# Kernel optimization log

Measured on AMD Instinct MI355X. Metric: run time of the kernel, lower is better.

Reference implementation:

```python
import jax, jax.numpy as jnp
import numpy as np

EPS = 2e-05
N_H_RDG = 9   # lifting scale grid: h_j = 2**j, j=0..8
N_H_CROP = 3  # group-conv scale support: offsets 0,1,2 (dyadic index shifts)


def _scaled_kernel(w, h):
    """Resample base kernel w [O, I, K] (taps on integers centered at 0) at
    coordinates x/h via linear interpolation -> [O, I, (K-1)*h+1], with the
    R+ Haar-measure normalization 1/h (psi_h(x) = psi(x/h)/h)."""
    K = w.shape[-1]
    Kh = (K - 1) * h + 1
    m = jnp.arange(K, dtype=jnp.float32) - K // 2
    x = (jnp.arange(Kh, dtype=jnp.float32) - Kh // 2) / h
    hat = jnp.maximum(0.0, 1.0 - jnp.abs(x[:, None] - m[None, :]))  # [Kh, K]
    return jnp.einsum('oim,xm->oix', w, hat) / h


def _conv1d_same(x, k):
    pad = (k.shape[-1] - 1) // 2
    return jax.lax.conv_general_dilated(
        x, k, window_strides=(1,), padding=[(pad, pad)],
        dimension_numbers=('NCH', 'OIH', 'NCH'))


def _pool_r1(x, stride):
    # max pool over the spatial (last) axis only: kernel 4, pad 1 each side
    return jax.lax.reduce_window(
        x, -jnp.inf, jax.lax.max,
        window_dimensions=(1, 1, 1, 4), window_strides=(1, 1, 1, stride),
        padding=((0, 0), (0, 0), (0, 0), (1, 1)))


def _bn(x, g, b):
    # BatchNorm2d over [B, C, H_scale, L], training-mode batch stats
    mu = jnp.mean(x, axis=(0, 2, 3), keepdims=True)
    var = jnp.var(x, axis=(0, 2, 3), keepdims=True)
    return (x - mu) * jax.lax.rsqrt(var + EPS) * g[None, :, None, None] + b[None, :, None, None]


def _forward(x, w1, w2, w3, g1, b1, g2, b2, g3, b3, fw1, fb1, fw2, fb2, fw3, fb3):
    B = x.shape[0]
    # --- c1: GConvRdG lifting, scales h_j = 2**j, j=0..8 ---
    out = jnp.stack([_conv1d_same(x, _scaled_kernel(w1, 2 ** j))
                     for j in range(N_H_RDG)], axis=2)      # [B,16,9,16]
    out = _bn(jax.nn.relu(_pool_r1(out, 2)), g1, b1)        # [B,16,9,8]
    # --- c2: GConvGG, h_crop=True: out scale j uses in scales j..j+2 ---
    O2, I2 = w2.shape[0], w2.shape[1]
    w2r = w2.reshape(O2, I2 * N_H_CROP, 3)
    H2 = out.shape[2] - (N_H_CROP - 1)  # 7
    out = jnp.stack([
        _conv1d_same(out[:, :, j:j + N_H_CROP, :].reshape(B, I2 * N_H_CROP, -1),
                     _scaled_kernel(w2r, 2 ** j))
        for j in range(H2)], axis=2)                        # [B,32,7,8]
    out = _bn(jax.nn.relu(_pool_r1(out, 2)), g2, b2)        # [B,32,7,4]
    # --- c3: GConvGG with 1x1 spatial kernel ---
    w3s = w3[:, :, :, 0]  # [64,32,3]
    H3 = out.shape[2] - (N_H_CROP - 1)  # 5
    out = jnp.stack([
        jnp.einsum('oik,bikl->bol', w3s, out[:, :, j:j + N_H_CROP, :]) / (2.0 ** j)
        for j in range(H3)], axis=2)                        # [B,64,5,4]
    out = _bn(jax.nn.relu(_pool_r1(out, 4)), g3, b3)        # [B,64,5,1]
    # --- MLP head (dropout is identity in eval) ---
    out = out.reshape(B, -1)                                # [B,320]
    out = out @ fw1.T + fb1
    out = out @ fw2.T + fb2
    return out @ fw3.T + fb3                                # [B,17]


def setup_inputs() -> dict:
    key = jax.random.key(0)
    ks = jax.random.split(key, 7)
    B = 4096
    x = jax.random.normal(ks[0], (B, 6, 16), dtype=jnp.float32)
    w1 = jax.random.normal(ks[1], (16, 6, 7), dtype=jnp.float32) * (6 * 7) ** -0.5
    w2 = jax.random.normal(ks[2], (32, 16, 3, 3), dtype=jnp.float32) * (16 * 3 * 3) ** -0.5
    w3 = jax.random.normal(ks[3], (64, 32, 3, 1), dtype=jnp.float32) * (32 * 3) ** -0.5
    fw1 = jax.random.normal(ks[4], (16, 320), dtype=jnp.float32) * 320 ** -0.5
    fw2 = jax.random.normal(ks[5], (16, 16), dtype=jnp.float32) * 16 ** -0.5
    fw3 = jax.random.normal(ks[6], (17, 16), dtype=jnp.float32) * 16 ** -0.5
    return {
        'x': x, 'w1': w1, 'w2': w2, 'w3': w3,
        'g1': jnp.ones(16), 'b1': jnp.zeros(16),
        'g2': jnp.ones(32), 'b2': jnp.zeros(32),
        'g3': jnp.ones(64), 'b3': jnp.zeros(64),
        'fw1': fw1, 'fb1': jnp.zeros(16),
        'fw2': fw2, 'fb2': jnp.zeros(16),
        'fw3': fw3, 'fb3': jnp.zeros(17),
    }


def reference(x, w1, w2, w3, g1, b1, g2, b2, g3, b3, fw1, fb1, fw2, fb2, fw3, fb3):
    return _forward(x, w1, w2, w3, g1, b1, g2, b2, g3, b3, fw1, fb1, fw2, fb2, fw3, fb3)
```

## Files before the change

### kernel.cpp

```cpp
#include <hip/hip_runtime.h>

#define EPS 2e-5f

using short8  = __attribute__((ext_vector_type(8))) short;
using floatx4 = __attribute__((ext_vector_type(4))) float;

static __device__ inline unsigned short f2bf(float f) {
    unsigned u = __float_as_uint(f);
    u += 0x7fffu + ((u >> 16) & 1u);
    return (unsigned short)(u >> 16);
}
static __device__ inline float bf2f(short s) {
    return __uint_as_float(((unsigned)(unsigned short)s) << 16);
}
static __device__ inline short8 scale8(short8 v, float sc) {
    short8 r;
    #pragma unroll
    for (int e = 0; e < 8; ++e) r[e] = (short)f2bf(bf2f(v[e]) * sc);
    return r;
}


__global__ void __launch_bounds__(256) kSa(const float* __restrict__ w1,
                                           unsigned short* __restrict__ W1f,
                                           float* __restrict__ stats) {
    int gid = blockIdx.x * 256 + threadIdx.x;
    if (gid < 256) stats[gid] = 0.f;
    int j  = gid / 24576;
    int r  = gid % 24576;
    int T  = r / 1536;
    int r2 = r % 1536;
    int ks = r2 / 512;
    int r3 = r2 % 512;
    int ln = r3 >> 3, e = r3 & 7;
    int n  = T * 16 + (ln & 15);
    int kk = ks * 32 + (ln >> 4) * 8 + e;
    int o = n >> 4, t = n & 15;
    int i = kk >> 4, s = kk & 15;
    int h = 1 << j;
    int d = s - t;
    float val = 0.f;
    if (d >= -3 * h && d <= 3 * h) {
        float df = (float)d / (float)h;
        #pragma unroll
        for (int m = 0; m < 7; ++m) {
            float hat = fmaxf(0.f, 1.f - fabsf(df - (float)(m - 3)));
            val += w1[(o * 6 + i) * 7 + m] * hat;
        }
        val /= (float)h;
    }
    W1f[gid] = f2bf(val);
}

__global__ void __launch_bounds__(256) k1(const float* __restrict__ x,
                                          const unsigned short* __restrict__ W1f,
                                          const float* __restrict__ w2,
                                          const float* __restrict__ w3,
                                          const float* __restrict__ fw1,
                                          unsigned short* __restrict__ p1,
                                          unsigned short* __restrict__ W2r,
                                          float* __restrict__ S,
                                          float* __restrict__ W3fF,
                                          float* __restrict__ W1rF,
                                          float* __restrict__ stats1, int B) {
    __shared__ float z[32 * 276];
    __shared__ float lsS[256], lsQ[256];
    int tid = threadIdx.x;

    if (blockIdx.y == 9) {
        int base = blockIdx.x * 256 + tid;
        for (int g = base; g < 688128; g += 32768) {
            int fs = g >> 9;
            int ln = (g >> 3) & 63, e = g & 7;
            int j  = fs / 192;
            int rm = fs % 192;
            int T  = rm / 12, ks = rm % 12;
            int col = T * 16 + (ln & 15);
            int k   = ks * 32 + (ln >> 4) * 8 + e;
            int o = col >> 3, t = col & 7;
            int ic = k >> 3, s = k & 7;
            int i = ic / 3, c = ic % 3;
            int h = 1 << j;
            int d = s - t;
            float raw = 0.f;
            if (d >= -h && d <= h) {
                float df = (float)d / (float)h;
                #pragma unroll
                for (int m = 0; m < 3; ++m) {
                    float hat = fmaxf(0.f, 1.f - fabsf(df - (float)(m - 1)));
                    raw += w2[((o * 16 + i) * 3 + c) * 3 + m] * hat;
                }
                raw /= (float)h;
            }
            W2r[g] = f2bf(raw);
        }
        for (int g = base; g < 28672; g += 32768) {
            int j = g >> 12;
            int r = g & 4095;
            int i = r >> 8;
            int col = r & 255;
            int o = col >> 3, t = col & 7;
            int h = 1 << j;
            float acc = 0.f;
            #pragma unroll
            for (int c = 0; c < 3; ++c) {
                const float* wr = &w2[((o * 16 + i) * 3 + c) * 3];
                #pragma unroll
                for (int s = 0; s < 8; ++s) {
                    int d = s - t;
                    if (d >= -h && d <= h) {
                        float df = (float)d / (float)h;
                        float raw = 0.f;
                        #pragma unroll
                        for (int m = 0; m < 3; ++m) {
                            float hat = fmaxf(0.f, 1.f - fabsf(df - (float)(m - 1)));
                            raw += wr[m] * hat;
                        }
                        acc += raw / (float)h;
                    }
                }
            }
            S[g] = acc;
        }
        for (int g = base; g < 6144; g += 32768) {
            int e = g & 7, ln = (g >> 3) & 63, fo = g >> 9;
            int kf = fo >> 2, og = fo & 3;
            int o = og * 16 + (ln & 15);
            int i = (ln >> 4) * 8 + e;
            W3fF[g] = w3[(o * 32 + i) * 3 + kf];
        }
        for (int g = base; g < 5120; g += 32768) {
            int e = g & 7, ln = (g >> 3) & 63, fo = g >> 9;
            int jj = fo >> 1, ks = fo & 1;
            int n = ln & 15;
            int oo = ks * 32 + (ln >> 4) * 8 + e;
            W1rF[g] = fw1[n * 320 + oo * 5 + jj];
        }
        return;
    }

    int j = blockIdx.y;
    int wav = tid >> 6, lane = tid & 63;
    int quad = lane >> 4, l15 = lane & 15;
    int msub = wav & 1, nh = wav >> 1;
    int b0 = blockIdx.x * 32;
    floatx4 acc[8];
    #pragma unroll
    for (int T = 0; T < 8; ++T) acc[T] = floatx4{0.f, 0.f, 0.f, 0.f};
    const float* xr = x + (size_t)(b0 + msub * 16 + l15) * 96;
    const short8* Bj = (const short8*)W1f + (size_t)(j * 16) * 3 * 64;
    #pragma unroll
    for (int ks = 0; ks < 3; ++ks) {
        int k0 = ks * 32 + quad * 8;
        floatx4 v0 = *(const floatx4*)(xr + k0);
        floatx4 v1 = *(const floatx4*)(xr + k0 + 4);
        short8 a;
        #pragma unroll
        for (int e = 0; e < 4; ++e) {
            a[e]     = (short)f2bf(v0[e]);
            a[e + 4] = (short)f2bf(v1[e]);
        }
        #pragma unroll
        for (int T = 0; T < 8; ++T) {
            short8 b = Bj[((nh * 8 + T) * 3 + ks) * 64 + lane];
            acc[T] = __builtin_amdgcn_mfma_f32_16x16x32_bf16(a, b, acc[T], 0, 0, 0);
        }
    }
    #pragma unroll
    for (int T = 0; T < 8; ++T) {
        int col = (nh * 8 + T) * 16 + l15;
        int rb  = msub * 16 + quad * 4;
        #pragma unroll
        for (int r = 0; r < 4; ++r) z[(rb + r) * 276 + col] = acc[T][r];
    }
    __syncthreads();
    float psum = 0.f, pss = 0.f;
    #pragma unroll
    for (int i = 0; i < 2; ++i) {
        int u = tid + 256 * i;
        int row = u >> 4, o = u & 15;
        const float* zr = &z[row * 276 + o * 16];
        floatx4 q0 = ((const floatx4*)zr)[0];
        floatx4 q1 = ((const floatx4*)zr)[1];
        floatx4 q2 = ((const floatx4*)zr)[2];
        floatx4 q3 = ((const floatx4*)zr)[3];
        float t[16] = {q0[0], q0[1], q0[2], q0[3], q1[0], q1[1], q1[2], q1[3],
                       q2[0], q2[1], q2[2], q2[3], q3[0], q3[1], q3[2], q3[3]};
        short8 pk;
        #pragma unroll
        for (int tp = 0; tp < 8; ++tp) {
            int lo = (tp == 0) ? 0 : 2 * tp - 1;
            int hi = (tp == 7) ? 15 : 2 * tp + 2;
            float m = t[lo];
            for (int tt = lo + 1; tt <= hi; ++tt) m = fmaxf(m, t[tt]);
            m = fmaxf(m, 0.f);
            pk[tp] = (short)f2bf(m);
            psum += m; pss += m * m;
        }
        *(short8*)(p1 + ((size_t)j * B + b0 + row) * 128 + o * 8) = pk;
    }
    lsS[(tid & 15) * 16 + (tid >> 4)] = psum;
    lsQ[(tid & 15) * 16 + (tid >> 4)] = pss;
    __syncthreads();
    if (tid < 32) {
        int o = tid & 15;
        const float* src = (tid < 16) ? lsS : lsQ;
        float s = 0.f;
        #pragma unroll
        for (int g = 0; g < 16; ++g) s += src[o * 16 + g];
        atomicAdd(&stats1[(tid < 16 ? 0 : 16) + o], s);
    }
}

__global__ void __launch_bounds__(256) k2(const unsigned short* __restrict__ p1,
                                          const unsigned short* __restrict__ W2r,
                                          const float* __restrict__ S,
                                          const float* __restrict__ g1,
                                          const float* __restrict__ b1,
                                          const float* __restrict__ stats1,
                                          unsigned short* __restrict__ p2s,
                                          float* __restrict__ stats2,
                                          float invN1, int B) {
    __shared__ float z[32 * 260];
    __shared__ float lsS[512], lsQ[512];
    __shared__ float a1s[16], d1s[16], bias2L[256];
    int tid = threadIdx.x, j = blockIdx.y;
    int wav = tid >> 6, lane = tid & 63;
    int quad = lane >> 4, l15 = lane & 15;
    int nh = wav & 1, mp = wav >> 1;
    int b0 = blockIdx.x * 64, m0 = b0 + mp * 32;
    if (tid < 16) {
        float mu  = stats1[tid] * invN1;
        float var = stats1[16 + tid] * invN1 - mu * mu;
        float rs  = rsqrtf(var + EPS);
        a1s[tid] = g1[tid] * rs;
        d1s[tid] = b1[tid] - mu * a1s[tid];
    }
    __syncthreads();
    {
        float s = 0.f;
        const float* Sj = S + (size_t)j * 4096;
        #pragma unroll
        for (int i = 0; i < 16; ++i) s = fmaf(d1s[i], Sj[i * 256 + tid], s);
        bias2L[tid] = s;
    }
    __syncthreads();
    float biasv[8];
    #pragma unroll
    for (int T = 0; T < 8; ++T) biasv[T] = bias2L[(nh * 8 + T) * 16 + l15];
    floatx4 acc[2][8];
    #pragma unroll
    for (int mi = 0; mi < 2; ++mi)
        #pragma unroll
        for (int T = 0; T < 8; ++T) acc[mi][T] = floatx4{0.f, 0.f, 0.f, 0.f};
    const short8* Bj = (const short8*)W2r + (size_t)(j * 16) * 12 * 64;
    #pragma unroll
    for (int ks = 0; ks < 12; ++ks) {
        int icq = ks * 4 + quad;
        int i = icq / 3, c = icq - i * 3;
        float a1v = a1s[i];
        const unsigned short* ap = p1 + ((size_t)(j + c) * B + m0 + l15) * 128 + i * 8;
        short8 a0 = scale8(*(const short8*)ap, a1v);
        short8 a1 = scale8(*(const short8*)(ap + 2048), a1v);
        #pragma unroll
        for (int T = 0; T < 8; ++T) {
            short8 b = Bj[((nh * 8 + T) * 12 + ks) * 64 + lane];
            acc[0][T] = __builtin_amdgcn_mfma_f32_16x16x32_bf16(a0, b, acc[0][T], 0, 0, 0);
            acc[1][T] = __builtin_amdgcn_mfma_f32_16x16x32_bf16(a1, b, acc[1][T], 0, 0, 0);
        }
    }
    float psum[2] = {0.f, 0.f}, pss[2] = {0.f, 0.f};
    for (int pass = 0; pass < 2; ++pass) {
        __syncthreads();
        if (mp == pass) {
            #pragma unroll
            for (int T = 0; T < 8; ++T) {
                int col = (nh * 8 + T) * 16 + l15;
                #pragma unroll
                for (int mi = 0; mi < 2; ++mi) {
                    int rb = mi * 16 + quad * 4;
                    #pragma unroll
                    for (int r = 0; r < 4; ++r)
                        z[(rb + r) * 260 + col] = acc[mi][T][r] + biasv[T];
                }
            }
        }
        __syncthreads();
        #pragma unroll
        for (int i2 = 0; i2 < 2; ++i2) {
            int u = tid + 256 * i2;
            int opr = u & 15, row = u >> 4;
            const float* zr = &z[row * 260 + opr * 16];
            floatx4 q0 = ((const floatx4*)zr)[0];
            floatx4 q1 = ((const floatx4*)zr)[1];
            floatx4 q2 = ((const floatx4*)zr)[2];
            floatx4 q3 = ((const floatx4*)zr)[3];
            float ta[8] = {q0[0], q0[1], q0[2], q0[3], q1[0], q1[1], q1[2], q1[3]};
            float tb[8] = {q2[0], q2[1], q2[2], q2[3], q3[0], q3[1], q3[2], q3[3]};
            int rowg = pass * 32 + row;
            #pragma unroll
            for (int tp = 0; tp < 4; ++tp) {
                int lo = (tp == 0) ? 0 : 2 * tp - 1;
                int hi = (tp == 3) ? 7 : 2 * tp + 2;
                float m0v = ta[lo], m1v = tb[lo];
                for (int tt = lo + 1; tt <= hi; ++tt) {
                    m0v = fmaxf(m0v, ta[tt]); m1v = fmaxf(m1v, tb[tt]);
                }
                m0v = fmaxf(m0v, 0.f); m1v = fmaxf(m1v, 0.f);
                psum[0] += m0v; pss[0] += m0v * m0v;
                psum[1] += m1v; pss[1] += m1v * m1v;
                unsigned pk = (unsigned)f2bf(m0v) | ((unsigned)f2bf(m1v) << 16);
                *(unsigned*)(p2s + ((size_t)(j * 4 + tp) * B + b0 + rowg) * 32
                             + opr * 2) = pk;
            }
        }
    }
    {
        int o0 = 2 * (tid & 15), g = tid >> 4;
        lsS[o0 * 16 + g] = psum[0]; lsS[(o0 + 1) * 16 + g] = psum[1];
        lsQ[o0 * 16 + g] = pss[0];  lsQ[(o0 + 1) * 16 + g] = pss[1];
    }
    __syncthreads();
    if (tid < 64) {
        int o = tid & 31;
        const float* src = (tid < 32) ? lsS : lsQ;
        float s = 0.f;
        #pragma unroll
        for (int g = 0; g < 16; ++g) s += src[o * 16 + g];
        atomicAdd(&stats2[(tid < 32 ? 0 : 32) + o], s);
    }
}

__global__ void __launch_bounds__(256) k3(const unsigned short* __restrict__ p2s,
                                          const float* __restrict__ W3fF,
                                          const float* __restrict__ g2,
                                          const float* __restrict__ b2,
                                          const float* __restrict__ stats2,
                                          unsigned short* __restrict__ act3,
                                          float* __restrict__ stats3,
                                          float invN2, int B) {
    __shared__ unsigned short atile[32][72];
    __shared__ float lsS[1024], lsQ[1024];
    int tid = threadIdx.x, j = blockIdx.y, b0 = blockIdx.x * 32;
    int og = tid >> 6, lane = tid & 63;
    int quad = lane >> 4, l15 = lane & 15;
    int i0 = quad * 8;
    floatx4 sm0 = *(const floatx4*)&stats2[i0];
    floatx4 sm1 = *(const floatx4*)&stats2[i0 + 4];
    floatx4 sq0 = *(const floatx4*)&stats2[32 + i0];
    floatx4 sq1 = *(const floatx4*)&stats2[32 + i0 + 4];
    floatx4 gg0 = *(const floatx4*)&g2[i0];
    floatx4 gg1 = *(const floatx4*)&g2[i0 + 4];
    floatx4 bv0 = *(const floatx4*)&b2[i0];
    floatx4 bv1 = *(const floatx4*)&b2[i0 + 4];
    float a2v[8], d2v[8];
    #pragma unroll
    for (int e = 0; e < 4; ++e) {
        float mu = sm0[e] * invN2;
        float var = sq0[e] * invN2 - mu * mu;
        float rs = rsqrtf(var + EPS);
        a2v[e] = gg0[e] * rs; d2v[e] = bv0[e] - mu * a2v[e];
        mu = sm1[e] * invN2;
        var = sq1[e] * invN2 - mu * mu;
        rs = rsqrtf(var + EPS);
        a2v[e + 4] = gg1[e] * rs; d2v[e + 4] = bv1[e] - mu * a2v[e + 4];
    }
    float biasacc = 0.f;
    short8 af[3];
    #pragma unroll
    for (int kf = 0; kf < 3; ++kf) {
        const float* wp = &W3fF[((size_t)(kf * 4 + og) * 64 + lane) * 8];
        floatx4 w0 = ((const floatx4*)wp)[0];
        floatx4 w1 = ((const floatx4*)wp)[1];
        float wr[8] = {w0[0], w0[1], w0[2], w0[3], w1[0], w1[1], w1[2], w1[3]};
        short8 v;
        #pragma unroll
        for (int e = 0; e < 8; ++e) {
            v[e] = (short)f2bf(wr[e] * a2v[e]);
            biasacc = fmaf(wr[e], d2v[e], biasacc);
        }
        af[kf] = v;
    }
    biasacc += __shfl_xor(biasacc, 16, 64);
    biasacc += __shfl_xor(biasacc, 32, 64);
    float brow[4];
    #pragma unroll
    for (int r = 0; r < 4; ++r) brow[r] = __shfl(biasacc, quad * 4 + r, 64);
    float inv = 1.f / (float)(1 << j);
    float psum[4] = {0.f, 0.f, 0.f, 0.f}, pss[4] = {0.f, 0.f, 0.f, 0.f};
    #pragma unroll
    for (int bt = 0; bt < 2; ++bt) {
        int bb = b0 + bt * 16;
        floatx4 aL0 = {0.f, 0.f, 0.f, 0.f};
        floatx4 aL1 = {0.f, 0.f, 0.f, 0.f};
        floatx4 aL2 = {0.f, 0.f, 0.f, 0.f};
        #pragma unroll
        for (int c = 0; c < 3; ++c) {
            const unsigned short* base =
                p2s + ((size_t)((j + c) * 4) * B + bb + l15) * 32 + quad * 8;
            short8 f0 = *(const short8*)base;
            short8 f1 = *(const short8*)(base + (size_t)B * 32);
            short8 f2v = *(const short8*)(base + (size_t)2 * B * 32);
            aL0 = __builtin_amdgcn_mfma_f32_16x16x32_bf16(af[c], f0, aL0, 0, 0, 0);
            aL1 = __builtin_amdgcn_mfma_f32_16x16x32_bf16(af[c], f1, aL1, 0, 0, 0);
            aL2 = __builtin_amdgcn_mfma_f32_16x16x32_bf16(af[c], f2v, aL2, 0, 0, 0);
        }
        #pragma unroll
        for (int r = 0; r < 4; ++r) {
            float vm = fmaxf(fmaxf(aL0[r], aL1[r]), aL2[r]);
            float v  = fmaxf((vm + brow[r]) * inv, 0.f);
            atile[bt * 16 + l15][og * 16 + quad * 4 + r] = f2bf(v);
            psum[r] += v; pss[r] += v * v;
        }
    }
    #pragma unroll
    for (int r = 0; r < 4; ++r) {
        lsS[(og * 16 + quad * 4 + r) * 16 + l15] = psum[r];
        lsQ[(og * 16 + quad * 4 + r) * 16 + l15] = pss[r];
    }
    __syncthreads();
    {
        int row = tid >> 3, oct = tid & 7;
        *(short8*)(act3 + ((size_t)j * B + b0 + row) * 64 + oct * 8) =
            *(const short8*)&atile[row][oct * 8];
    }
    if (tid < 128) {
        int oo = tid & 63;
        const float* src = (tid < 64) ? lsS : lsQ;
        float s = 0.f;
        #pragma unroll
        for (int g = 0; g < 16; ++g) s += src[oo * 16 + g];
        atomicAdd(&stats3[(tid < 64 ? 0 : 64) + oo], s);
    }
}

__global__ void __launch_bounds__(128) k4(const unsigned short* __restrict__ act3,
                                          const float* __restrict__ W1rF,
                                          const float* __restrict__ g3,
                                          const float* __restrict__ b3,
                                          const float* __restrict__ stats3,
                                          const float* __restrict__ fw1,
                                          const float* __restrict__ fb1,
                                          const float* __restrict__ fw2,
                                          const float* __restrict__ fb2,
                                          const float* __restrict__ fw3,
                                          const float* __restrict__ fb3,
                                          float* __restrict__ out,
                                          float invN3, int B) {
    __shared__ float a3s[64], d3s[64];
    __shared__ float fw2s[256], fw3s[272], fb2s[16], fb3s[17], fb1f[16], tmp[4][16];
    __shared__ float hbuf[2][16][17];
    int tid = threadIdx.x;
    int wav = tid >> 6, lane = tid & 63;
    int quad = lane >> 4, l15 = lane & 15;
    if (tid < 64) {
        float mu  = stats3[tid] * invN3;
        float var = stats3[64 + tid] * invN3 - mu * mu;
        float rs  = rsqrtf(var + EPS);
        float a   = g3[tid] * rs;
        a3s[tid] = a;
        d3s[tid] = b3[tid] - mu * a;
    }
    if (tid < 16) fb2s[tid] = fb2[tid];
    if (tid < 17) fb3s[tid] = fb3[tid];
    #pragma unroll
    for (int u = 0; u < 2; ++u) fw2s[tid + u * 128] = fw2[tid + u * 128];
    for (int idx = tid; idx < 272; idx += 128) fw3s[idx] = fw3[idx];
    __syncthreads();
    if (tid < 64) {
        int f = tid & 15, ch = tid >> 4;
        float s = 0.f;
        for (int u = 0; u < 80; ++u) {
            int n = ch * 80 + u;
            s = fmaf(fw1[f * 320 + n], d3s[n / 5], s);
        }
        tmp[ch][f] = s;
    }
    float a3v[2][8];
    #pragma unroll
    for (int ks = 0; ks < 2; ++ks)
        #pragma unroll
        for (int e = 0; e < 8; ++e) a3v[ks][e] = a3s[ks * 32 + quad * 8 + e];
    int mt = blockIdx.x * 2 + wav;
    floatx4 acc = {0.f, 0.f, 0.f, 0.f};
    #pragma unroll
    for (int jj = 0; jj < 5; ++jj)
        #pragma unroll
        for (int ks = 0; ks < 2; ++ks) {
            short8 a = *(const short8*)(act3 +
                ((size_t)jj * B + mt * 16 + l15) * 64 + ks * 32 + quad * 8);
            const float* wp = &W1rF[((size_t)(jj * 2 + ks) * 64 + lane) * 8];
            floatx4 w0 = ((const floatx4*)wp)[0];
            floatx4 w1 = ((const floatx4*)wp)[1];
            short8 b;
            #pragma unroll
            for (int e = 0; e < 4; ++e) {
                b[e]     = (short)f2bf(w0[e] * a3v[ks][e]);
                b[e + 4] = (short)f2bf(w1[e] * a3v[ks][e + 4]);
            }
            acc = __builtin_amdgcn_mfma_f32_16x16x32_bf16(a, b, acc, 0, 0, 0);
        }
    __syncthreads();
    if (tid < 16) fb1f[tid] = fb1[tid] + tmp[0][tid] + tmp[1][tid]
                            + tmp[2][tid] + tmp[3][tid];
    __syncthreads();
    #pragma unroll
    for (int r = 0; r < 4; ++r) hbuf[wav][quad * 4 + r][l15] = acc[r] + fb1f[l15];
    __syncthreads();
    if (lane < 16) {
        int row = l15;
        float hv[16];
        #pragma unroll
        for (int n = 0; n < 16; ++n) hv[n] = hbuf[wav][row][n];
        float h2[16];
        #pragma unroll
        for (int f2 = 0; f2 < 16; ++f2) {
            float s = fb2s[f2];
            #pragma unroll
            for (int n = 0; n < 16; ++n) s = fmaf(fw2s[f2 * 16 + n], hv[n], s);
            h2[f2] = s;
        }
        float* orow = out + (size_t)(mt * 16 + row) * 17;
        #pragma unroll
        for (int f3 = 0; f3 < 17; ++f3) {
            float s = fb3s[f3];
            #pragma unroll
            for (int n = 0; n < 16; ++n) s = fmaf(fw3s[f3 * 16 + n], h2[n], s);
            orow[f3] = s;
        }
    }
}

extern "C" void kernel_launch(void* const* d_in, const int* in_sizes, int n_in,
                              void* d_out, int out_size, void* d_ws, size_t ws_size,
                              hipStream_t stream) {
    (void)n_in; (void)out_size; (void)ws_size;
    const float* x   = (const float*)d_in[0];
    const float* w1  = (const float*)d_in[1];
    const float* w2  = (const float*)d_in[2];
    const float* w3  = (const float*)d_in[3];
    const float* g1  = (const float*)d_in[4];
    const float* b1  = (const float*)d_in[5];
    const float* g2  = (const float*)d_in[6];
    const float* b2  = (const float*)d_in[7];
    const float* g3  = (const float*)d_in[8];
    const float* b3  = (const float*)d_in[9];
    const float* fw1 = (const float*)d_in[10];
    const float* fb1 = (const float*)d_in[11];
    const float* fw2 = (const float*)d_in[12];
    const float* fb2 = (const float*)d_in[13];
    const float* fw3 = (const float*)d_in[14];
    const float* fb3 = (const float*)d_in[15];
    float* out = (float*)d_out;

    int B = in_sizes[0] / 96;

    char* wsb = (char*)d_ws;
    float*          stats = (float*)wsb;
    unsigned short* W1f   = (unsigned short*)(wsb + 1024);
    unsigned short* W2r   = W1f + 221184;
    float*          S     = (float*)(W2r + 688128);
    float*          W3fF  = S + 28672;
    float*          W1rF  = W3fF + 6144;
    unsigned short* p1    = (unsigned short*)(W1rF + 5120);
    unsigned short* p2s   = p1 + (size_t)9 * B * 128;
    unsigned short* act3  = p2s + (size_t)28 * B * 32;

    float* stats1 = stats;
    float* stats2 = stats + 32;
    float* stats3 = stats + 96;

    float invN1 = 1.f / (float)(B * 72);
    float invN2 = 1.f / (float)(B * 28);
    float invN3 = 1.f / (float)(B * 5);

    kSa<<<864, 256, 0, stream>>>(w1, W1f, stats);
    k1<<<dim3(B / 32, 10), 256, 0, stream>>>(x, W1f, w2, w3, fw1, p1, W2r, S,
                                             W3fF, W1rF, stats1, B);
    k2<<<dim3(B / 64, 7), 256, 0, stream>>>(p1, W2r, S, g1, b1, stats1, p2s, stats2,
                                            invN1, B);
    k3<<<dim3(B / 32, 5), 256, 0, stream>>>(p2s, W3fF, g2, b2, stats2, act3, stats3,
                                            invN2, B);
    k4<<<B / 32, 128, 0, stream>>>(act3, W1rF, g3, b3, stats3, fw1, fb1, fw2, fb2,
                                   fw3, fb3, out, invN3, B);
}
```

Before: 176.9 us.

## Replace LDS-staged pooling epilogues with in-register wave shuffles

In k1 and k2 the max-pool, ReLU and BN-statistics epilogue now reads neighbouring MFMA accumulator lanes through __shfl instead of staging the tile in large shared-memory buffers behind barriers. Per-channel sums are reduced with xor-shuffle trees. k3 writes its bf16 output directly and reduces its stats with shuffles and atomics instead of an LDS tile. Dropping the big LDS arrays and adding launch-bounds occupancy hints is meant to raise occupancy and remove barrier and LDS traffic. The trade-offs are extra shuffle instructions, narrower 4-byte scattered stores, and more global atomics in k3.

```diff
diff --git a/kernel.cpp b/kernel.cpp
--- a/kernel.cpp
+++ b/kernel.cpp
@@ -3,6 +3,7 @@
 #define EPS 2e-5f
 
 using short8  = __attribute__((ext_vector_type(8))) short;
+using short4v = __attribute__((ext_vector_type(4))) short;
 using floatx4 = __attribute__((ext_vector_type(4))) float;
 
 static __device__ inline unsigned short f2bf(float f) {
@@ -52,19 +53,18 @@
     W1f[gid] = f2bf(val);
 }
 
-__global__ void __launch_bounds__(256) k1(const float* __restrict__ x,
-                                          const unsigned short* __restrict__ W1f,
-                                          const float* __restrict__ w2,
-                                          const float* __restrict__ w3,
-                                          const float* __restrict__ fw1,
-                                          unsigned short* __restrict__ p1,
-                                          unsigned short* __restrict__ W2r,
-                                          float* __restrict__ S,
-                                          float* __restrict__ W3fF,
-                                          float* __restrict__ W1rF,
-                                          float* __restrict__ stats1, int B) {
-    __shared__ float z[32 * 276];
-    __shared__ float lsS[256], lsQ[256];
+__global__ void __launch_bounds__(256, 5) k1(const float* __restrict__ x,
+                                             const unsigned short* __restrict__ W1f,
+                                             const float* __restrict__ w2,
+                                             const float* __restrict__ w3,
+                                             const float* __restrict__ fw1,
+                                             unsigned short* __restrict__ p1,
+                                             unsigned short* __restrict__ W2r,
+                                             float* __restrict__ S,
+                                             float* __restrict__ W3fF,
+                                             float* __restrict__ W1rF,
+                                             float* __restrict__ stats1, int B) {
+    __shared__ float lsS[32], lsQ[32];
     int tid = threadIdx.x;
 
     if (blockIdx.y == 9) {
@@ -166,64 +166,68 @@
             acc[T] = __builtin_amdgcn_mfma_f32_16x16x32_bf16(a, b, acc[T], 0, 0, 0);
         }
     }
+    bool vld = (l15 == 0) || ((l15 & 1) && l15 <= 13);
+    bool pks = (l15 == 0) || (l15 == 3) || (l15 == 7) || (l15 == 11);
+    int tpp = (l15 + 2) >> 2;
+    int i1 = quad * 16 + ((l15 < 15) ? l15 + 1 : 15);
+    int i2 = quad * 16 + ((l15 < 14) ? l15 + 2 : 15);
+    int i3 = quad * 16 + ((l15 < 13) ? l15 + 3 : 15);
+    int prt = quad * 16 + l15 + ((l15 == 0) ? 1 : 2);
+    float psel = 0.f, qsel = 0.f;
     #pragma unroll
     for (int T = 0; T < 8; ++T) {
-        int col = (nh * 8 + T) * 16 + l15;
-        int rb  = msub * 16 + quad * 4;
-        #pragma unroll
-        for (int r = 0; r < 4; ++r) z[(rb + r) * 276 + col] = acc[T][r];
-    }
-    __syncthreads();
-    float psum = 0.f, pss = 0.f;
-    #pragma unroll
-    for (int i = 0; i < 2; ++i) {
-        int u = tid + 256 * i;
-        int row = u >> 4, o = u & 15;
-        const float* zr = &z[row * 276 + o * 16];
-        floatx4 q0 = ((const floatx4*)zr)[0];
-        floatx4 q1 = ((const floatx4*)zr)[1];
-        floatx4 q2 = ((const floatx4*)zr)[2];
-        floatx4 q3 = ((const floatx4*)zr)[3];
-        float t[16] = {q0[0], q0[1], q0[2], q0[3], q1[0], q1[1], q1[2], q1[3],
-                       q2[0], q2[1], q2[2], q2[3], q3[0], q3[1], q3[2], q3[3]};
-        short8 pk;
-        #pragma unroll
-        for (int tp = 0; tp < 8; ++tp) {
-            int lo = (tp == 0) ? 0 : 2 * tp - 1;
-            int hi = (tp == 7) ? 15 : 2 * tp + 2;
-            float m = t[lo];
-            for (int tt = lo + 1; tt <= hi; ++tt) m = fmaxf(m, t[tt]);
-            m = fmaxf(m, 0.f);
-            pk[tp] = (short)f2bf(m);
-            psum += m; pss += m * m;
-        }
-        *(short8*)(p1 + ((size_t)j * B + b0 + row) * 128 + o * 8) = pk;
-    }
-    lsS[(tid & 15) * 16 + (tid >> 4)] = psum;
-    lsQ[(tid & 15) * 16 + (tid >> 4)] = pss;
-    __syncthreads();
-    if (tid < 32) {
-        int o = tid & 15;
-        const float* src = (tid < 16) ? lsS : lsQ;
-        float s = 0.f;
-        #pragma unroll
-        for (int g = 0; g < 16; ++g) s += src[o * 16 + g];
-        atomicAdd(&stats1[(tid < 16 ? 0 : 16) + o], s);
-    }
-}
-
-__global__ void __launch_bounds__(256) k2(const unsigned short* __restrict__ p1,
-                                          const unsigned short* __restrict__ W2r,
-                                          const float* __restrict__ S,
-                                          const float* __restrict__ g1,
-                                          const float* __restrict__ b1,
-                                          const float* __restrict__ stats1,
-                                          unsigned short* __restrict__ p2s,
-                                          float* __restrict__ stats2,
-                                          float invN1, int B) {
-    __shared__ float z[32 * 260];
-    __shared__ float lsS[512], lsQ[512];
+        int o = nh * 8 + T;
+        float pT = 0.f, qT = 0.f;
+        #pragma unroll
+        for (int r = 0; r < 4; ++r) {
+            float v = acc[T][r];
+            float d1 = __shfl(v, i1, 64);
+            float d2 = __shfl(v, i2, 64);
+            float d3 = __shfl(v, i3, 64);
+            float m3 = fmaxf(fmaxf(v, d1), d2);
+            float m4 = fmaxf(m3, d3);
+            float m = fmaxf((l15 == 0 || l15 == 13) ? m3 : m4, 0.f);
+            float mq = __shfl(m, prt, 64);
+            if (vld) { pT += m; qT += m * m; }
+            if (pks) {
+                unsigned pk = (unsigned)f2bf(m) | ((unsigned)f2bf(mq) << 16);
+                int row = b0 + msub * 16 + quad * 4 + r;
+                *(unsigned*)(p1 + ((size_t)j * B + row) * 128 + o * 8 + tpp * 2) = pk;
+            }
+        }
+        float ps = pT, qs = qT;
+        ps += __shfl_xor(ps, 1, 64);  qs += __shfl_xor(qs, 1, 64);
+        ps += __shfl_xor(ps, 2, 64);  qs += __shfl_xor(qs, 2, 64);
+        ps += __shfl_xor(ps, 4, 64);  qs += __shfl_xor(qs, 4, 64);
+        ps += __shfl_xor(ps, 8, 64);  qs += __shfl_xor(qs, 8, 64);
+        ps += __shfl_xor(ps, 16, 64); qs += __shfl_xor(qs, 16, 64);
+        ps += __shfl_xor(ps, 32, 64); qs += __shfl_xor(qs, 32, 64);
+        if (lane == T) { psel = ps; qsel = qs; }
+    }
+    if (lane < 8) {
+        int o = nh * 8 + lane;
+        lsS[o * 2 + msub] = psel;
+        lsQ[o * 2 + msub] = qsel;
+    }
+    __syncthreads();
+    if (tid < 16) atomicAdd(&stats1[tid], lsS[tid * 2] + lsS[tid * 2 + 1]);
+    else if (tid < 32) {
+        int o = tid - 16;
+        atomicAdd(&stats1[16 + o], lsQ[o * 2] + lsQ[o * 2 + 1]);
+    }
+}
+
+__global__ void __launch_bounds__(256, 4) k2(const unsigned short* __restrict__ p1,
+                                             const unsigned short* __restrict__ W2r,
+                                             const float* __restrict__ S,
+                                             const float* __restrict__ g1,
+                                             const float* __restrict__ b1,
+                                             const float* __restrict__ stats1,
+                                             unsigned short* __restrict__ p2s,
+                                             float* __restrict__ stats2,
+                                             float invN1, int B) {
     __shared__ float a1s[16], d1s[16], bias2L[256];
+    __shared__ float lsS[64], lsQ[64];
     int tid = threadIdx.x, j = blockIdx.y;
     int wav = tid >> 6, lane = tid & 63;
     int quad = lane >> 4, l15 = lane & 15;
@@ -269,78 +273,68 @@
             acc[1][T] = __builtin_amdgcn_mfma_f32_16x16x32_bf16(a1, b, acc[1][T], 0, 0, 0);
         }
     }
-    float psum[2] = {0.f, 0.f}, pss[2] = {0.f, 0.f};
-    for (int pass = 0; pass < 2; ++pass) {
-        __syncthreads();
-        if (mp == pass) {
+    int gl = l15 & 7, gh = l15 >> 3;
+    int gb = quad * 16 + gh * 8;
+    int i1 = gb + ((gl < 7) ? gl + 1 : 7);
+    int i2 = gb + ((gl < 6) ? gl + 2 : 7);
+    int i3 = gb + ((gl < 5) ? gl + 3 : 7);
+    int prt = quad * 16 + 8 + gl;
+    bool vld = (gl == 0) || (gl == 1) || (gl == 3) || (gl == 5);
+    bool pks = vld && (gh == 0);
+    int tp = (gl + 1) >> 1;
+    #pragma unroll
+    for (int T = 0; T < 8; ++T) {
+        float pT = 0.f, qT = 0.f;
+        #pragma unroll
+        for (int mi = 0; mi < 2; ++mi) {
             #pragma unroll
-            for (int T = 0; T < 8; ++T) {
-                int col = (nh * 8 + T) * 16 + l15;
-                #pragma unroll
-                for (int mi = 0; mi < 2; ++mi) {
-                    int rb = mi * 16 + quad * 4;
-                    #pragma unroll
-                    for (int r = 0; r < 4; ++r)
-                        z[(rb + r) * 260 + col] = acc[mi][T][r] + biasv[T];
+            for (int r = 0; r < 4; ++r) {
+                float v = acc[mi][T][r] + biasv[T];
+                float d1 = __shfl(v, i1, 64);
+                float d2 = __shfl(v, i2, 64);
+                float d3 = __shfl(v, i3, 64);
+                float m3 = fmaxf(fmaxf(v, d1), d2);
+                float m4 = fmaxf(m3, d3);
+                float m = fmaxf((gl == 1 || gl == 3) ? m4 : m3, 0.f);
+                float mq = __shfl(m, prt, 64);
+                if (vld) { pT += m; qT += m * m; }
+                if (pks) {
+                    unsigned pk = (unsigned)f2bf(m) | ((unsigned)f2bf(mq) << 16);
+                    int rowg = mp * 32 + mi * 16 + quad * 4 + r;
+                    *(unsigned*)(p2s + ((size_t)(j * 4 + tp) * B + b0 + rowg) * 32
+                                 + (nh * 8 + T) * 2) = pk;
                 }
             }
         }
-        __syncthreads();
-        #pragma unroll
-        for (int i2 = 0; i2 < 2; ++i2) {
-            int u = tid + 256 * i2;
-            int opr = u & 15, row = u >> 4;
-            const float* zr = &z[row * 260 + opr * 16];
-            floatx4 q0 = ((const floatx4*)zr)[0];
-            floatx4 q1 = ((const floatx4*)zr)[1];
-            floatx4 q2 = ((const floatx4*)zr)[2];
-            floatx4 q3 = ((const floatx4*)zr)[3];
-            float ta[8] = {q0[0], q0[1], q0[2], q0[3], q1[0], q1[1], q1[2], q1[3]};
-            float tb[8] = {q2[0], q2[1], q2[2], q2[3], q3[0], q3[1], q3[2], q3[3]};
-            int rowg = pass * 32 + row;
-            #pragma unroll
-            for (int tp = 0; tp < 4; ++tp) {
-                int lo = (tp == 0) ? 0 : 2 * tp - 1;
-                int hi = (tp == 3) ? 7 : 2 * tp + 2;
-                float m0v = ta[lo], m1v = tb[lo];
-                for (int tt = lo + 1; tt <= hi; ++tt) {
-                    m0v = fmaxf(m0v, ta[tt]); m1v = fmaxf(m1v, tb[tt]);
-                }
-                m0v = fmaxf(m0v, 0.f); m1v = fmaxf(m1v, 0.f);
-                psum[0] += m0v; pss[0] += m0v * m0v;
-                psum[1] += m1v; pss[1] += m1v * m1v;
-                unsigned pk = (unsigned)f2bf(m0v) | ((unsigned)f2bf(m1v) << 16);
-                *(unsigned*)(p2s + ((size_t)(j * 4 + tp) * B + b0 + rowg) * 32
-                             + opr * 2) = pk;
-            }
-        }
-    }
-    {
-        int o0 = 2 * (tid & 15), g = tid >> 4;
-        lsS[o0 * 16 + g] = psum[0]; lsS[(o0 + 1) * 16 + g] = psum[1];
-        lsQ[o0 * 16 + g] = pss[0];  lsQ[(o0 + 1) * 16 + g] = pss[1];
-    }
-    __syncthreads();
-    if (tid < 64) {
-        int o = tid & 31;
-        const float* src = (tid < 32) ? lsS : lsQ;
-        float s = 0.f;
-        #pragma unroll
-        for (int g = 0; g < 16; ++g) s += src[o * 16 + g];
-        atomicAdd(&stats2[(tid < 32 ? 0 : 32) + o], s);
-    }
-}
-
-__global__ void __launch_bounds__(256) k3(const unsigned short* __restrict__ p2s,
-                                          const float* __restrict__ W3fF,
-                                          const float* __restrict__ g2,
-                                          const float* __restrict__ b2,
-                                          const float* __restrict__ stats2,
-                                          unsigned short* __restrict__ act3,
-                                          float* __restrict__ stats3,
-                                          float invN2, int B) {
-    __shared__ unsigned short atile[32][72];
-    __shared__ float lsS[1024], lsQ[1024];
+        float ps = pT, qs = qT;
+        ps += __shfl_xor(ps, 1, 64);  qs += __shfl_xor(qs, 1, 64);
+        ps += __shfl_xor(ps, 2, 64);  qs += __shfl_xor(qs, 2, 64);
+        ps += __shfl_xor(ps, 4, 64);  qs += __shfl_xor(qs, 4, 64);
+        ps += __shfl_xor(ps, 16, 64); qs += __shfl_xor(qs, 16, 64);
+        ps += __shfl_xor(ps, 32, 64); qs += __shfl_xor(qs, 32, 64);
+        if (quad == 0 && gl == 0) {
+            int o = (nh * 8 + T) * 2 + gh;
+            lsS[o * 2 + mp] = ps;
+            lsQ[o * 2 + mp] = qs;
+        }
+    }
+    __syncthreads();
+    if (tid < 32) {
+        atomicAdd(&stats2[tid], lsS[tid * 2] + lsS[tid * 2 + 1]);
+    } else if (tid < 64) {
+        int o = tid - 32;
+        atomicAdd(&stats2[32 + o], lsQ[o * 2] + lsQ[o * 2 + 1]);
+    }
+}
+
+__global__ void __launch_bounds__(256, 5) k3(const unsigned short* __restrict__ p2s,
+                                             const float* __restrict__ W3fF,
+                                             const float* __restrict__ g2,
+                                             const float* __restrict__ b2,
+                                             const float* __restrict__ stats2,
+                                             unsigned short* __restrict__ act3,
+                                             float* __restrict__ stats3,
+                                             float invN2, int B) {
     int tid = threadIdx.x, j = blockIdx.y, b0 = blockIdx.x * 32;
     int og = tid >> 6, lane = tid & 63;
     int quad = lane >> 4, l15 = lane & 15;
@@ -405,32 +399,28 @@
             aL1 = __builtin_amdgcn_mfma_f32_16x16x32_bf16(af[c], f1, aL1, 0, 0, 0);
             aL2 = __builtin_amdgcn_mfma_f32_16x16x32_bf16(af[c], f2v, aL2, 0, 0, 0);
         }
+        short4v pk;
         #pragma unroll
         for (int r = 0; r < 4; ++r) {
             float vm = fmaxf(fmaxf(aL0[r], aL1[r]), aL2[r]);
             float v  = fmaxf((vm + brow[r]) * inv, 0.f);
-            atile[bt * 16 + l15][og * 16 + quad * 4 + r] = f2bf(v);
+            pk[r] = (short)f2bf(v);
             psum[r] += v; pss[r] += v * v;
         }
+        *(short4v*)(act3 + ((size_t)j * B + bb + l15) * 64 + og * 16 + quad * 4) = pk;
     }
     #pragma unroll
     for (int r = 0; r < 4; ++r) {
-        lsS[(og * 16 + quad * 4 + r) * 16 + l15] = psum[r];
-        lsQ[(og * 16 + quad * 4 + r) * 16 + l15] = pss[r];
-    }
-    __syncthreads();
-    {
-        int row = tid >> 3, oct = tid & 7;
-        *(short8*)(act3 + ((size_t)j * B + b0 + row) * 64 + oct * 8) =
-            *(const short8*)&atile[row][oct * 8];
-    }
-    if (tid < 128) {
-        int oo = tid & 63;
-        const float* src = (tid < 64) ? lsS : lsQ;
-        float s = 0.f;
-        #pragma unroll
-        for (int g = 0; g < 16; ++g) s += src[oo * 16 + g];
-        atomicAdd(&stats3[(tid < 64 ? 0 : 64) + oo], s);
+        float ps = psum[r], qs = pss[r];
+        ps += __shfl_xor(ps, 1, 64); qs += __shfl_xor(qs, 1, 64);
+        ps += __shfl_xor(ps, 2, 64); qs += __shfl_xor(qs, 2, 64);
+        ps += __shfl_xor(ps, 4, 64); qs += __shfl_xor(qs, 4, 64);
+        ps += __shfl_xor(ps, 8, 64); qs += __shfl_xor(qs, 8, 64);
+        if (l15 == 0) {
+            int ch = og * 16 + quad * 4 + r;
+            atomicAdd(&stats3[ch], ps);
+            atomicAdd(&stats3[64 + ch], qs);
+        }
     }
 }
 
```

New measurement: 231.9 us. +31.1%, slower.
